# Kernel tuning notes

Measured on AMD Instinct MI355X. Metric: run time of the kernel, lower is better.

## Reference

```python
import jax, jax.numpy as jnp
import numpy as np

N = 50000      # nodes
E = 800000     # edges
IN = 128       # in_channels
H = 128        # hidden_channels
OUT = 40       # out_channels (classes)
EPS = 1e-5     # LayerNorm eps


def _glorot(key, fan_in, fan_out):
    lim = np.sqrt(6.0 / (fan_in + fan_out)).astype(np.float32)
    return jax.random.uniform(key, (fan_in, fan_out), jnp.float32, -lim, lim)


def setup_inputs() -> dict:
    key = jax.random.key(0)
    ks = jax.random.split(key, 8)
    x = jax.random.normal(ks[0], (N, IN), jnp.float32)
    edge_index = jax.random.randint(ks[1], (2, E), 0, N, jnp.int32)
    return {
        "x": x,
        "W0": _glorot(ks[2], IN, H), "b0": jnp.zeros((H,), jnp.float32),
        "W1": _glorot(ks[3], H, H),  "b1": jnp.zeros((H,), jnp.float32),
        "W2": _glorot(ks[4], H, OUT), "b2": jnp.zeros((OUT,), jnp.float32),
        "ln1_g": jnp.ones((H,), jnp.float32), "ln1_b": jnp.zeros((H,), jnp.float32),
        "ln2_g": jnp.ones((H,), jnp.float32), "ln2_b": jnp.zeros((H,), jnp.float32),
        "edge_index": edge_index,
    }


def reference(x, W0, b0, W1, b1, W2, b2, ln1_g, ln1_b, ln2_g, ln2_b, edge_index):
    # GCN normalization with self-loops: A_hat = D^-1/2 (A + I) D^-1/2
    self_idx = jnp.arange(N, dtype=edge_index.dtype)
    src = jnp.concatenate([edge_index[0], self_idx])  # [E+N]
    dst = jnp.concatenate([edge_index[1], self_idx])
    deg = jax.ops.segment_sum(jnp.ones_like(src, jnp.float32), dst, num_segments=N)
    dinv = jax.lax.rsqrt(deg)  # deg >= 1 thanks to self-loops
    norm = dinv[src] * dinv[dst]  # [E+N]

    def conv(h, W, b):
        h = h @ W                                  # [N, F] dense GEMM
        msg = h[src] * norm[:, None]               # gather + scale [E+N, F]
        return jax.ops.segment_sum(msg, dst, num_segments=N) + b

    def layernorm(h, g, b):
        mu = jnp.mean(h, axis=-1, keepdims=True)
        var = jnp.mean(jnp.square(h - mu), axis=-1, keepdims=True)
        return (h - mu) * jax.lax.rsqrt(var + EPS) * g + b

    # layer 0 (note: original uses lns[i+1], so lns[0] is never applied)
    h = jax.nn.relu(layernorm(conv(x, W0, b0), ln1_g, ln1_b))
    # dropout is identity in eval mode
    h = jax.nn.relu(layernorm(conv(h, W1, b1), ln2_g, ln2_b))
    h = conv(h, W2, b2)
    return jax.nn.log_softmax(h, axis=-1)
```

## Files before the change

### kernel.cpp

```cpp
#include <hip/hip_runtime.h>
#include <math.h>

typedef __attribute__((ext_vector_type(8))) short bf16x8;
typedef __attribute__((ext_vector_type(4))) float f32x4;
typedef unsigned short u16;

static __device__ __forceinline__ u16 f2bf(float f) {
    unsigned u = __float_as_uint(f);
    unsigned r = (u + 0x7fff + ((u >> 16) & 1)) >> 16;
    return (u16)r;
}
static __device__ __forceinline__ float bf2f(u16 h) {
    return __uint_as_float(((unsigned)h) << 16);
}
static __device__ __forceinline__ float pk_lo(unsigned u) { return __uint_as_float(u << 16); }
static __device__ __forceinline__ float pk_hi(unsigned u) { return __uint_as_float(u & 0xffff0000u); }

__global__ void zero_int_k(int* __restrict__ p, int n) {
    int i = blockIdx.x * 256 + threadIdx.x;
    if (i < n) p[i] = 0;
}
__global__ void count_rank_k(const int* __restrict__ dst, int* __restrict__ counts,
                             int* __restrict__ rank, int e) {
    int i = blockIdx.x * 256 + threadIdx.x;
    if (i < e) rank[i] = atomicAdd(&counts[dst[i]], 1);
}
__global__ __launch_bounds__(1024) void scan1_k(const int* __restrict__ counts,
                                                int* __restrict__ offs,
                                                int* __restrict__ bsum,
                                                float* __restrict__ dinv, int n) {
    __shared__ int ws[16];
    int tid = threadIdx.x;
    int i = blockIdx.x * 1024 + tid;
    int lane = tid & 63, w = tid >> 6;
    int c = (i < n) ? counts[i] : 0;
    if (i < n) dinv[i] = rsqrtf((float)c + 1.0f);
    int s = c;
#pragma unroll
    for (int o = 1; o < 64; o <<= 1) { int t = __shfl_up(s, o); if (lane >= o) s += t; }
    if (lane == 63) ws[w] = s;
    __syncthreads();
    if (w == 0) {
        int x = (lane < 16) ? ws[lane] : 0;
#pragma unroll
        for (int o = 1; o < 16; o <<= 1) { int t = __shfl_up(x, o); if (lane >= o) x += t; }
        if (lane < 16) ws[lane] = x;
    }
    __syncthreads();
    int base = (w > 0) ? ws[w - 1] : 0;
    int incl = base + s;
    if (i < n) offs[i + 1] = incl;
    if (tid == 1023) bsum[blockIdx.x] = incl;
}
__global__ void scan2_k(int* __restrict__ bsum, int nb) {
    int lane = threadIdx.x;
    int v = (lane < nb) ? bsum[lane] : 0;
#pragma unroll
    for (int o = 1; o < 64; o <<= 1) { int t = __shfl_up(v, o); if (lane >= o) v += t; }
    if (lane < nb) bsum[lane] = v;
}
__global__ void scan3_k(int* __restrict__ offs, const int* __restrict__ bsum, int n) {
    int i = blockIdx.x * 256 + threadIdx.x;
    if (i == 0) offs[0] = 0;
    if (i < n) {
        int b = i >> 10;
        offs[i + 1] += (b > 0) ? bsum[b - 1] : 0;
    }
}
__global__ void fill2_k(const int* __restrict__ src, const int* __restrict__ dst,
                        const int* __restrict__ rank, const int* __restrict__ offs,
                        int* __restrict__ csr, int e) {
    int i = blockIdx.x * 256 + threadIdx.x;
    if (i < e) csr[offs[dst[i]] + rank[i]] = src[i];
}

__global__ void pack_all_k(const float* __restrict__ W0, const float* __restrict__ W1,
                           const float* __restrict__ W2,
                           u16* __restrict__ w0hi, u16* __restrict__ w0lo,
                           u16* __restrict__ w1hi, u16* __restrict__ w1lo,
                           u16* __restrict__ w2hi, u16* __restrict__ w2lo) {
    int i = blockIdx.x * 256 + threadIdx.x;
    const float* W; u16 *hi, *lo; int COLS, cin, idx;
    if (i < 16384)      { W = W0; hi = w0hi; lo = w0lo; COLS = 128; cin = 128; idx = i; }
    else if (i < 32768) { W = W1; hi = w1hi; lo = w1lo; COLS = 128; cin = 128; idx = i - 16384; }
    else if (i < 40960) { W = W2; hi = w2hi; lo = w2lo; COLS = 64;  cin = 40;  idx = i - 32768; }
    else return;
    int k = idx / COLS, col = idx % COLS;
    float v = (col < cin) ? W[k * cin + col] : 0.f;
    u16 h = f2bf(v);
    u16 l = f2bf(v - bf2f(h));
    int ct = col >> 4, ks = k >> 5, ln = (col & 15) + (((k >> 3) & 3) << 4), j = k & 7;
    int pos = (((ct * 4 + ks) * 64 + ln) << 3) + j;
    hi[pos] = h; lo[pos] = l;
}

template<int COLS>
__global__ __launch_bounds__(256) void mfma_gemm_f32a_k(const float* __restrict__ A,
                                                        const u16* __restrict__ Whi,
                                                        const u16* __restrict__ Wlo,
                                                        const float* __restrict__ dinv,
                                                        u16* __restrict__ C, int nrows) {
    int wave = threadIdx.x >> 6, lane = threadIdx.x & 63;
    int r0 = blockIdx.x * 64 + wave * 16;
    int arow = min(r0 + (lane & 15), nrows - 1);
    int kbase = (lane >> 4) * 8;

    bf16x8 ahi[4], alo[4];
#pragma unroll
    for (int ks = 0; ks < 4; ++ks) {
        const float* ap = &A[(long)arow * 128 + ks * 32 + kbase];
        float4 f0 = *(const float4*)ap;
        float4 f1 = *(const float4*)(ap + 4);
        float fv[8] = {f0.x, f0.y, f0.z, f0.w, f1.x, f1.y, f1.z, f1.w};
#pragma unroll
        for (int j = 0; j < 8; ++j) {
            u16 h = f2bf(fv[j]);
            ahi[ks][j] = (short)h;
            alo[ks][j] = (short)f2bf(fv[j] - bf2f(h));
        }
    }
    float dscale[4];
#pragma unroll
    for (int r = 0; r < 4; ++r) {
        int orow = r0 + (lane >> 4) * 4 + r;
        dscale[r] = (orow < nrows) ? dinv[orow] : 0.f;
    }
#pragma unroll
    for (int ct = 0; ct < COLS / 16; ct += 2) {
        f32x4 acc0 = {0.f, 0.f, 0.f, 0.f}, acc1 = {0.f, 0.f, 0.f, 0.f};
#pragma unroll
        for (int ks = 0; ks < 4; ++ks) {
            int fo0 = ((ct * 4 + ks) * 64 + lane) * 8;
            int fo1 = (((ct + 1) * 4 + ks) * 64 + lane) * 8;
            bf16x8 bhi0 = *(const bf16x8*)&Whi[fo0];
            bf16x8 blo0 = *(const bf16x8*)&Wlo[fo0];
            bf16x8 bhi1 = *(const bf16x8*)&Whi[fo1];
            bf16x8 blo1 = *(const bf16x8*)&Wlo[fo1];
            acc0 = __builtin_amdgcn_mfma_f32_16x16x32_bf16(ahi[ks], bhi0, acc0, 0, 0, 0);
            acc1 = __builtin_amdgcn_mfma_f32_16x16x32_bf16(ahi[ks], bhi1, acc1, 0, 0, 0);
            acc0 = __builtin_amdgcn_mfma_f32_16x16x32_bf16(alo[ks], bhi0, acc0, 0, 0, 0);
            acc1 = __builtin_amdgcn_mfma_f32_16x16x32_bf16(alo[ks], bhi1, acc1, 0, 0, 0);
            acc0 = __builtin_amdgcn_mfma_f32_16x16x32_bf16(ahi[ks], blo0, acc0, 0, 0, 0);
            acc1 = __builtin_amdgcn_mfma_f32_16x16x32_bf16(ahi[ks], blo1, acc1, 0, 0, 0);
        }
#pragma unroll
        for (int r = 0; r < 4; ++r) {
            int orow = r0 + (lane >> 4) * 4 + r;
            if (orow < nrows) {
                C[(long)orow * COLS + ct * 16 + (lane & 15)] = f2bf(acc0[r] * dscale[r]);
                C[(long)orow * COLS + (ct + 1) * 16 + (lane & 15)] = f2bf(acc1[r] * dscale[r]);
            }
        }
    }
}

template<int COLS>
__global__ __launch_bounds__(256) void mfma_gemm_bf16a_k(const u16* __restrict__ A,
                                                         const u16* __restrict__ Whi,
                                                         const u16* __restrict__ Wlo,
                                                         const float* __restrict__ dinv,
                                                         u16* __restrict__ C, int nrows) {
    int wave = threadIdx.x >> 6, lane = threadIdx.x & 63;
    int r0 = blockIdx.x * 64 + wave * 16;
    int arow = min(r0 + (lane & 15), nrows - 1);
    int kbase = (lane >> 4) * 8;

    bf16x8 a[4];
#pragma unroll
    for (int ks = 0; ks < 4; ++ks)
        a[ks] = *(const bf16x8*)&A[(long)arow * 128 + ks * 32 + kbase];

    float dscale[4];
#pragma unroll
    for (int r = 0; r < 4; ++r) {
        int orow = r0 + (lane >> 4) * 4 + r;
        dscale[r] = (orow < nrows) ? dinv[orow] : 0.f;
    }
#pragma unroll
    for (int ct = 0; ct < COLS / 16; ct += 2) {
        f32x4 acc0 = {0.f, 0.f, 0.f, 0.f}, acc1 = {0.f, 0.f, 0.f, 0.f};
#pragma unroll
        for (int ks = 0; ks < 4; ++ks) {
            int fo0 = ((ct * 4 + ks) * 64 + lane) * 8;
            int fo1 = (((ct + 1) * 4 + ks) * 64 + lane) * 8;
            bf16x8 bhi0 = *(const bf16x8*)&Whi[fo0];
            bf16x8 blo0 = *(const bf16x8*)&Wlo[fo0];
            bf16x8 bhi1 = *(const bf16x8*)&Whi[fo1];
            bf16x8 blo1 = *(const bf16x8*)&Wlo[fo1];
            acc0 = __builtin_amdgcn_mfma_f32_16x16x32_bf16(a[ks], bhi0, acc0, 0, 0, 0);
            acc1 = __builtin_amdgcn_mfma_f32_16x16x32_bf16(a[ks], bhi1, acc1, 0, 0, 0);
            acc0 = __builtin_amdgcn_mfma_f32_16x16x32_bf16(a[ks], blo0, acc0, 0, 0, 0);
            acc1 = __builtin_amdgcn_mfma_f32_16x16x32_bf16(a[ks], blo1, acc1, 0, 0, 0);
        }
#pragma unroll
        for (int r = 0; r < 4; ++r) {
            int orow = r0 + (lane >> 4) * 4 + r;
            if (orow < nrows) {
                C[(long)orow * COLS + ct * 16 + (lane & 15)] = f2bf(acc0[r] * dscale[r]);
                C[(long)orow * COLS + (ct + 1) * 16 + (lane & 15)] = f2bf(acc1[r] * dscale[r]);
            }
        }
    }
}

__global__ __launch_bounds__(256) void agg_ln_relu_k(const u16* __restrict__ Cs,
                                                     const int* __restrict__ offs,
                                                     const int* __restrict__ csr,
                                                     const float* __restrict__ dinv,
                                                     const float* __restrict__ bias,
                                                     const float* __restrict__ g,
                                                     const float* __restrict__ b,
                                                     u16* __restrict__ out, int n) {
    int wid = (blockIdx.x * 256 + threadIdx.x) >> 6;
    int lane = threadIdx.x & 63;
    if (wid >= n) return;
    const unsigned* C2 = (const unsigned*)Cs;
    unsigned su = C2[(long)wid * 64 + lane];
    float ax = pk_lo(su), ay = pk_hi(su), bx2 = 0.f, by2 = 0.f;
    int beg = offs[wid], end = offs[wid + 1];
    int j = beg;
    while (j < end) {
        int take = min(64, end - j);
        int myidx = (lane < take) ? csr[j + lane] : 0;
        int k = 0;
        for (; k + 8 <= take; k += 8) {
            int i0 = __shfl(myidx, k),     i1 = __shfl(myidx, k + 1);
            int i2 = __shfl(myidx, k + 2), i3 = __shfl(myidx, k + 3);
            int i4 = __shfl(myidx, k + 4), i5 = __shfl(myidx, k + 5);
            int i6 = __shfl(myidx, k + 6), i7 = __shfl(myidx, k + 7);
            unsigned u0 = C2[(long)i0 * 64 + lane], u1 = C2[(long)i1 * 64 + lane];
            unsigned u2 = C2[(long)i2 * 64 + lane], u3 = C2[(long)i3 * 64 + lane];
            unsigned u4 = C2[(long)i4 * 64 + lane], u5 = C2[(long)i5 * 64 + lane];
            unsigned u6 = C2[(long)i6 * 64 + lane], u7 = C2[(long)i7 * 64 + lane];
            ax += pk_lo(u0) + pk_lo(u1) + pk_lo(u2) + pk_lo(u3);
            ay += pk_hi(u0) + pk_hi(u1) + pk_hi(u2) + pk_hi(u3);
            bx2 += pk_lo(u4) + pk_lo(u5) + pk_lo(u6) + pk_lo(u7);
            by2 += pk_hi(u4) + pk_hi(u5) + pk_hi(u6) + pk_hi(u7);
        }
        for (; k < take; ++k) {
            int i0 = __shfl(myidx, k);
            unsigned u0 = C2[(long)i0 * 64 + lane];
            ax += pk_lo(u0); ay += pk_hi(u0);
        }
        j += take;
    }
    float w = dinv[wid];
    float2 bia = ((const float2*)bias)[lane];
    float t0 = (ax + bx2) * w + bia.x;
    float t1 = (ay + by2) * w + bia.y;
    float s = t0 + t1;
#pragma unroll
    for (int off = 32; off; off >>= 1) s += __shfl_xor(s, off);
    float mu = s * (1.f / 128.f);
    float d0 = t0 - mu, d1 = t1 - mu;
    float v = d0 * d0 + d1 * d1;
#pragma unroll
    for (int off = 32; off; off >>= 1) v += __shfl_xor(v, off);
    float rstd = rsqrtf(v * (1.f / 128.f) + 1e-5f);
    float2 gv = ((const float2*)g)[lane];
    float2 bv = ((const float2*)b)[lane];
    float y0 = fmaxf(0.f, d0 * rstd * gv.x + bv.x);
    float y1 = fmaxf(0.f, d1 * rstd * gv.y + bv.y);
    ((unsigned*)out)[(long)wid * 64 + lane] = ((unsigned)f2bf(y1) << 16) | f2bf(y0);
}

__global__ __launch_bounds__(256) void agg_lsm_k(const u16* __restrict__ Cs,
                                                 const int* __restrict__ offs,
                                                 const int* __restrict__ csr,
                                                 const float* __restrict__ dinv,
                                                 const float* __restrict__ b2,
                                                 float* __restrict__ out, int n) {
    int wid = (blockIdx.x * 256 + threadIdx.x) >> 6;
    int lane = threadIdx.x & 63;
    if (wid >= n) return;
    float aa = bf2f(Cs[(long)wid * 64 + lane]), ab = 0.f;
    int beg = offs[wid], end = offs[wid + 1];
    int j = beg;
    while (j < end) {
        int take = min(64, end - j);
        int myidx = (lane < take) ? csr[j + lane] : 0;
        int k = 0;
        for (; k + 8 <= take; k += 8) {
            int i0 = __shfl(myidx, k),     i1 = __shfl(myidx, k + 1);
            int i2 = __shfl(myidx, k + 2), i3 = __shfl(myidx, k + 3);
            int i4 = __shfl(myidx, k + 4), i5 = __shfl(myidx, k + 5);
            int i6 = __shfl(myidx, k + 6), i7 = __shfl(myidx, k + 7);
            float v0 = bf2f(Cs[(long)i0 * 64 + lane]), v1 = bf2f(Cs[(long)i1 * 64 + lane]);
            float v2 = bf2f(Cs[(long)i2 * 64 + lane]), v3 = bf2f(Cs[(long)i3 * 64 + lane]);
            float v4 = bf2f(Cs[(long)i4 * 64 + lane]), v5 = bf2f(Cs[(long)i5 * 64 + lane]);
            float v6 = bf2f(Cs[(long)i6 * 64 + lane]), v7 = bf2f(Cs[(long)i7 * 64 + lane]);
            aa += v0 + v1 + v2 + v3;
            ab += v4 + v5 + v6 + v7;
        }
        for (; k < take; ++k) {
            int i0 = __shfl(myidx, k);
            aa += bf2f(Cs[(long)i0 * 64 + lane]);
        }
        j += take;
    }
    float v = (lane < 40) ? (aa + ab) * dinv[wid] + b2[lane] : -INFINITY;
    float m = v;
#pragma unroll
    for (int off = 32; off; off >>= 1) m = fmaxf(m, __shfl_xor(m, off));
    float e = (lane < 40) ? expf(v - m) : 0.f;
    float s = e;
#pragma unroll
    for (int off = 32; off; off >>= 1) s += __shfl_xor(s, off);
    float r = v - m - logf(s);
    if (lane < 40) out[(long)wid * 40 + lane] = r;
}

extern "C" void kernel_launch(void* const* d_in, const int* in_sizes, int n_in,
                              void* d_out, int out_size, void* d_ws, size_t ws_size,
                              hipStream_t stream) {
    const float* x    = (const float*)d_in[0];
    const float* W0   = (const float*)d_in[1];
    const float* b0   = (const float*)d_in[2];
    const float* W1   = (const float*)d_in[3];
    const float* b1   = (const float*)d_in[4];
    const float* W2   = (const float*)d_in[5];
    const float* b2   = (const float*)d_in[6];
    const float* ln1g = (const float*)d_in[7];
    const float* ln1b = (const float*)d_in[8];
    const float* ln2g = (const float*)d_in[9];
    const float* ln2b = (const float*)d_in[10];
    const int*   ei   = (const int*)d_in[11];

    const int N = in_sizes[0] / 128;
    const int E = in_sizes[11] / 2;
    const int* esrc = ei;
    const int* edst = ei + E;
    float* out = (float*)d_out;

    const int Npad = ((N + 255) / 256) * 256;

    int* counts = (int*)d_ws;
    int* offs   = counts + Npad;
    int* rank   = offs + Npad;
    int* bsum   = rank + E;
    int* csr    = bsum + 64;
    float* dinv = (float*)(csr + E);
    u16* bufA   = (u16*)(dinv + Npad);
    u16* bufB   = bufA + (long)N * 128;
    u16* w0hi   = bufB + (long)N * 128;
    u16* w0lo   = w0hi + 16384;
    u16* w1hi   = w0lo + 16384;
    u16* w1lo   = w1hi + 16384;
    u16* w2hi   = w1lo + 16384;
    u16* w2lo   = w2hi + 8192;

    dim3 blk(256);
    int gN = (N + 255) / 256, gE = (E + 255) / 256;
    int nb1024 = (N + 1023) / 1024;

    zero_int_k<<<gN, blk, 0, stream>>>(counts, N);
    count_rank_k<<<gE, blk, 0, stream>>>(edst, counts, rank, E);
    scan1_k<<<nb1024, 1024, 0, stream>>>(counts, offs, bsum, dinv, N);
    scan2_k<<<1, 64, 0, stream>>>(bsum, nb1024);
    scan3_k<<<gN, blk, 0, stream>>>(offs, bsum, N);
    fill2_k<<<gE, blk, 0, stream>>>(esrc, edst, rank, offs, csr, E);

    pack_all_k<<<160, blk, 0, stream>>>(W0, W1, W2, w0hi, w0lo, w1hi, w1lo, w2hi, w2lo);

    int gG = (N + 63) / 64;
    mfma_gemm_f32a_k<128><<<gG, blk, 0, stream>>>(x, w0hi, w0lo, dinv, bufA, N);
    agg_ln_relu_k<<<(N + 3) / 4, blk, 0, stream>>>(bufA, offs, csr, dinv, b0, ln1g, ln1b, bufB, N);
    mfma_gemm_bf16a_k<128><<<gG, blk, 0, stream>>>(bufB, w1hi, w1lo, dinv, bufA, N);
    agg_ln_relu_k<<<(N + 3) / 4, blk, 0, stream>>>(bufA, offs, csr, dinv, b1, ln2g, ln2b, bufB, N);
    mfma_gemm_bf16a_k<64><<<gG, blk, 0, stream>>>(bufB, w2hi, w2lo, dinv, bufA, N);
    agg_lsm_k<<<(N + 3) / 4, blk, 0, stream>>>(bufA, offs, csr, dinv, b2, out, N);
}
```

Baseline: 213.9 us.

## Slice GEMM outputs by column, aggregate per slice, fuse LayerNorm into next GEMM

GEMM outputs are now stored in column-sliced layout (8 slices of 16 or 8 bf16 columns), so that each aggregation block gathers only a narrow slice per neighbor. The goal is better cache locality for the random-access gather. LayerNorm, bias and ReLU move from the aggregation kernel into the prologue of the following GEMM, and a small kernel applies log-softmax at the end. CSR indices and ranks are shrunk to 16-bit to cut index traffic, which assumes N fits in 65536 (true for 50000). The aggregated sum is rounded to bf16 before normalization, which adds some rounding error.

```diff
diff --git a/kernel.cpp b/kernel.cpp
--- a/kernel.cpp
+++ b/kernel.cpp
@@ -4,6 +4,7 @@
 typedef __attribute__((ext_vector_type(8))) short bf16x8;
 typedef __attribute__((ext_vector_type(4))) float f32x4;
 typedef unsigned short u16;
+typedef unsigned int u32;
 
 static __device__ __forceinline__ u16 f2bf(float f) {
     unsigned u = __float_as_uint(f);
@@ -13,17 +14,17 @@
 static __device__ __forceinline__ float bf2f(u16 h) {
     return __uint_as_float(((unsigned)h) << 16);
 }
-static __device__ __forceinline__ float pk_lo(unsigned u) { return __uint_as_float(u << 16); }
-static __device__ __forceinline__ float pk_hi(unsigned u) { return __uint_as_float(u & 0xffff0000u); }
+static __device__ __forceinline__ float pk_lo(u32 u) { return __uint_as_float(u << 16); }
+static __device__ __forceinline__ float pk_hi(u32 u) { return __uint_as_float(u & 0xffff0000u); }
 
 __global__ void zero_int_k(int* __restrict__ p, int n) {
     int i = blockIdx.x * 256 + threadIdx.x;
     if (i < n) p[i] = 0;
 }
 __global__ void count_rank_k(const int* __restrict__ dst, int* __restrict__ counts,
-                             int* __restrict__ rank, int e) {
-    int i = blockIdx.x * 256 + threadIdx.x;
-    if (i < e) rank[i] = atomicAdd(&counts[dst[i]], 1);
+                             u16* __restrict__ rank, int e) {
+    int i = blockIdx.x * 256 + threadIdx.x;
+    if (i < e) rank[i] = (u16)atomicAdd(&counts[dst[i]], 1);
 }
 __global__ __launch_bounds__(1024) void scan1_k(const int* __restrict__ counts,
                                                 int* __restrict__ offs,
@@ -68,10 +69,10 @@
     }
 }
 __global__ void fill2_k(const int* __restrict__ src, const int* __restrict__ dst,
-                        const int* __restrict__ rank, const int* __restrict__ offs,
-                        int* __restrict__ csr, int e) {
-    int i = blockIdx.x * 256 + threadIdx.x;
-    if (i < e) csr[offs[dst[i]] + rank[i]] = src[i];
+                        const u16* __restrict__ rank, const int* __restrict__ offs,
+                        u16* __restrict__ csr, int e) {
+    int i = blockIdx.x * 256 + threadIdx.x;
+    if (i < e) csr[offs[dst[i]] + (int)rank[i]] = (u16)src[i];
 }
 
 __global__ void pack_all_k(const float* __restrict__ W0, const float* __restrict__ W1,
@@ -92,6 +93,13 @@
     int ct = col >> 4, ks = k >> 5, ln = (col & 15) + (((k >> 3) & 3) << 4), j = k & 7;
     int pos = (((ct * 4 + ks) * 64 + ln) << 3) + j;
     hi[pos] = h; lo[pos] = l;
+}
+
+template<int COLS>
+static __device__ __forceinline__ void store_slice(u16* C, int N, int row, int c, float v) {
+    constexpr int SH = (COLS == 128) ? 4 : 3;
+    constexpr int SC = 1 << SH;
+    C[((size_t)(c >> SH) * N + row) * SC + (c & (SC - 1))] = f2bf(v);
 }
 
 template<int COLS>
@@ -147,28 +155,70 @@
         for (int r = 0; r < 4; ++r) {
             int orow = r0 + (lane >> 4) * 4 + r;
             if (orow < nrows) {
-                C[(long)orow * COLS + ct * 16 + (lane & 15)] = f2bf(acc0[r] * dscale[r]);
-                C[(long)orow * COLS + (ct + 1) * 16 + (lane & 15)] = f2bf(acc1[r] * dscale[r]);
+                store_slice<COLS>(C, nrows, orow, ct * 16 + (lane & 15), acc0[r] * dscale[r]);
+                store_slice<COLS>(C, nrows, orow, (ct + 1) * 16 + (lane & 15), acc1[r] * dscale[r]);
             }
         }
     }
 }
 
 template<int COLS>
-__global__ __launch_bounds__(256) void mfma_gemm_bf16a_k(const u16* __restrict__ A,
-                                                         const u16* __restrict__ Whi,
-                                                         const u16* __restrict__ Wlo,
-                                                         const float* __restrict__ dinv,
-                                                         u16* __restrict__ C, int nrows) {
+__global__ __launch_bounds__(256) void gemm_ln_k(const u32* __restrict__ agg,
+                                                 const u16* __restrict__ Whi,
+                                                 const u16* __restrict__ Wlo,
+                                                 const float* __restrict__ dinv,
+                                                 const float* __restrict__ bias,
+                                                 const float* __restrict__ g,
+                                                 const float* __restrict__ b,
+                                                 u16* __restrict__ C, int nrows) {
     int wave = threadIdx.x >> 6, lane = threadIdx.x & 63;
     int r0 = blockIdx.x * 64 + wave * 16;
     int arow = min(r0 + (lane & 15), nrows - 1);
-    int kbase = (lane >> 4) * 8;
-
-    bf16x8 a[4];
+    int kb = lane >> 4;
+
+    const u32* ap = agg + (size_t)arow * 64 + kb * 4;
+    float dA = dinv[arow];
+    float tv[4][8];
+    float ssum = 0.f;
+#pragma unroll
+    for (int ks = 0; ks < 4; ++ks) {
+#pragma unroll
+        for (int w2 = 0; w2 < 4; ++w2) {
+            u32 u = ap[ks * 16 + w2];
+            int wi = ks * 16 + kb * 4 + w2;
+            float2 bi = ((const float2*)bias)[wi];
+            float t0 = pk_lo(u) * dA + bi.x;
+            float t1 = pk_hi(u) * dA + bi.y;
+            tv[ks][w2 * 2] = t0; tv[ks][w2 * 2 + 1] = t1;
+            ssum += t0 + t1;
+        }
+    }
+    ssum += __shfl_xor(ssum, 16);
+    ssum += __shfl_xor(ssum, 32);
+    float mu = ssum * (1.f / 128.f);
+    float ssq = 0.f;
 #pragma unroll
     for (int ks = 0; ks < 4; ++ks)
-        a[ks] = *(const bf16x8*)&A[(long)arow * 128 + ks * 32 + kbase];
+#pragma unroll
+        for (int j = 0; j < 8; ++j) { float d = tv[ks][j] - mu; ssq += d * d; }
+    ssq += __shfl_xor(ssq, 16);
+    ssq += __shfl_xor(ssq, 32);
+    float rstd = rsqrtf(ssq * (1.f / 128.f) + 1e-5f);
+
+    bf16x8 afr[4];
+#pragma unroll
+    for (int ks = 0; ks < 4; ++ks) {
+#pragma unroll
+        for (int w2 = 0; w2 < 4; ++w2) {
+            int wi = ks * 16 + kb * 4 + w2;
+            float2 gv = ((const float2*)g)[wi];
+            float2 bv = ((const float2*)b)[wi];
+            float y0 = fmaxf(0.f, (tv[ks][w2 * 2] - mu) * rstd * gv.x + bv.x);
+            float y1 = fmaxf(0.f, (tv[ks][w2 * 2 + 1] - mu) * rstd * gv.y + bv.y);
+            afr[ks][w2 * 2] = (short)f2bf(y0);
+            afr[ks][w2 * 2 + 1] = (short)f2bf(y1);
+        }
+    }
 
     float dscale[4];
 #pragma unroll
@@ -187,127 +237,86 @@
             bf16x8 blo0 = *(const bf16x8*)&Wlo[fo0];
             bf16x8 bhi1 = *(const bf16x8*)&Whi[fo1];
             bf16x8 blo1 = *(const bf16x8*)&Wlo[fo1];
-            acc0 = __builtin_amdgcn_mfma_f32_16x16x32_bf16(a[ks], bhi0, acc0, 0, 0, 0);
-            acc1 = __builtin_amdgcn_mfma_f32_16x16x32_bf16(a[ks], bhi1, acc1, 0, 0, 0);
-            acc0 = __builtin_amdgcn_mfma_f32_16x16x32_bf16(a[ks], blo0, acc0, 0, 0, 0);
-            acc1 = __builtin_amdgcn_mfma_f32_16x16x32_bf16(a[ks], blo1, acc1, 0, 0, 0);
+            acc0 = __builtin_amdgcn_mfma_f32_16x16x32_bf16(afr[ks], bhi0, acc0, 0, 0, 0);
+            acc1 = __builtin_amdgcn_mfma_f32_16x16x32_bf16(afr[ks], bhi1, acc1, 0, 0, 0);
+            acc0 = __builtin_amdgcn_mfma_f32_16x16x32_bf16(afr[ks], blo0, acc0, 0, 0, 0);
+            acc1 = __builtin_amdgcn_mfma_f32_16x16x32_bf16(afr[ks], blo1, acc1, 0, 0, 0);
         }
 #pragma unroll
         for (int r = 0; r < 4; ++r) {
             int orow = r0 + (lane >> 4) * 4 + r;
             if (orow < nrows) {
-                C[(long)orow * COLS + ct * 16 + (lane & 15)] = f2bf(acc0[r] * dscale[r]);
-                C[(long)orow * COLS + (ct + 1) * 16 + (lane & 15)] = f2bf(acc1[r] * dscale[r]);
+                store_slice<COLS>(C, nrows, orow, ct * 16 + (lane & 15), acc0[r] * dscale[r]);
+                store_slice<COLS>(C, nrows, orow, (ct + 1) * 16 + (lane & 15), acc1[r] * dscale[r]);
             }
         }
     }
 }
 
-__global__ __launch_bounds__(256) void agg_ln_relu_k(const u16* __restrict__ Cs,
-                                                     const int* __restrict__ offs,
-                                                     const int* __restrict__ csr,
-                                                     const float* __restrict__ dinv,
-                                                     const float* __restrict__ bias,
-                                                     const float* __restrict__ g,
-                                                     const float* __restrict__ b,
-                                                     u16* __restrict__ out, int n) {
+template<int WS>
+__global__ __launch_bounds__(256) void agg_slice_k(const u32* __restrict__ Csl,
+                                                   const int* __restrict__ offs,
+                                                   const u16* __restrict__ csr,
+                                                   u32* __restrict__ aggout, int n) {
+    int s = blockIdx.x & 7;
+    int node = (blockIdx.x >> 3) * 4 + (threadIdx.x >> 6);
+    if (node >= n) return;
+    int l = threadIdx.x & 63;
+    int w = l & (WS - 1);
+    int t = l / WS;
+    constexpr int SLOTS = 64 / WS;
+    const u32* C = Csl + (size_t)s * n * WS;
+    float ax = 0.f, ay = 0.f;
+    if (l < WS) {
+        u32 u = C[(size_t)node * WS + w];
+        ax = pk_lo(u); ay = pk_hi(u);
+    }
+    int beg = offs[node], end = offs[node + 1];
+    for (int j = beg; j < end; j += 64) {
+        int cnt = min(64, end - j);
+        int idx = (l < cnt) ? (int)csr[j + l] : 0;
+        for (int k = 0; k < cnt; k += SLOTS) {
+            int e = k + t;
+            int src = __shfl(idx, e);
+            if (e < cnt) {
+                u32 u = C[(size_t)src * WS + w];
+                ax += pk_lo(u); ay += pk_hi(u);
+            }
+        }
+    }
+#pragma unroll
+    for (int m = WS; m < 64; m <<= 1) {
+        ax += __shfl_xor(ax, m);
+        ay += __shfl_xor(ay, m);
+    }
+    if (l < WS)
+        aggout[(size_t)node * (8 * WS) + s * WS + w] = ((u32)f2bf(ay) << 16) | (u32)f2bf(ax);
+}
+
+__global__ __launch_bounds__(256) void lsm2_k(const u32* __restrict__ agg3,
+                                              const float* __restrict__ dinv,
+                                              const float* __restrict__ b2,
+                                              float* __restrict__ out, int n) {
     int wid = (blockIdx.x * 256 + threadIdx.x) >> 6;
     int lane = threadIdx.x & 63;
     if (wid >= n) return;
-    const unsigned* C2 = (const unsigned*)Cs;
-    unsigned su = C2[(long)wid * 64 + lane];
-    float ax = pk_lo(su), ay = pk_hi(su), bx2 = 0.f, by2 = 0.f;
-    int beg = offs[wid], end = offs[wid + 1];
-    int j = beg;
-    while (j < end) {
-        int take = min(64, end - j);
-        int myidx = (lane < take) ? csr[j + lane] : 0;
-        int k = 0;
-        for (; k + 8 <= take; k += 8) {
-            int i0 = __shfl(myidx, k),     i1 = __shfl(myidx, k + 1);
-            int i2 = __shfl(myidx, k + 2), i3 = __shfl(myidx, k + 3);
-            int i4 = __shfl(myidx, k + 4), i5 = __shfl(myidx, k + 5);
-            int i6 = __shfl(myidx, k + 6), i7 = __shfl(myidx, k + 7);
-            unsigned u0 = C2[(long)i0 * 64 + lane], u1 = C2[(long)i1 * 64 + lane];
-            unsigned u2 = C2[(long)i2 * 64 + lane], u3 = C2[(long)i3 * 64 + lane];
-            unsigned u4 = C2[(long)i4 * 64 + lane], u5 = C2[(long)i5 * 64 + lane];
-            unsigned u6 = C2[(long)i6 * 64 + lane], u7 = C2[(long)i7 * 64 + lane];
-            ax += pk_lo(u0) + pk_lo(u1) + pk_lo(u2) + pk_lo(u3);
-            ay += pk_hi(u0) + pk_hi(u1) + pk_hi(u2) + pk_hi(u3);
-            bx2 += pk_lo(u4) + pk_lo(u5) + pk_lo(u6) + pk_lo(u7);
-            by2 += pk_hi(u4) + pk_hi(u5) + pk_hi(u6) + pk_hi(u7);
-        }
-        for (; k < take; ++k) {
-            int i0 = __shfl(myidx, k);
-            unsigned u0 = C2[(long)i0 * 64 + lane];
-            ax += pk_lo(u0); ay += pk_hi(u0);
-        }
-        j += take;
-    }
-    float w = dinv[wid];
-    float2 bia = ((const float2*)bias)[lane];
-    float t0 = (ax + bx2) * w + bia.x;
-    float t1 = (ay + by2) * w + bia.y;
-    float s = t0 + t1;
-#pragma unroll
-    for (int off = 32; off; off >>= 1) s += __shfl_xor(s, off);
-    float mu = s * (1.f / 128.f);
-    float d0 = t0 - mu, d1 = t1 - mu;
-    float v = d0 * d0 + d1 * d1;
-#pragma unroll
-    for (int off = 32; off; off >>= 1) v += __shfl_xor(v, off);
-    float rstd = rsqrtf(v * (1.f / 128.f) + 1e-5f);
-    float2 gv = ((const float2*)g)[lane];
-    float2 bv = ((const float2*)b)[lane];
-    float y0 = fmaxf(0.f, d0 * rstd * gv.x + bv.x);
-    float y1 = fmaxf(0.f, d1 * rstd * gv.y + bv.y);
-    ((unsigned*)out)[(long)wid * 64 + lane] = ((unsigned)f2bf(y1) << 16) | f2bf(y0);
-}
-
-__global__ __launch_bounds__(256) void agg_lsm_k(const u16* __restrict__ Cs,
-                                                 const int* __restrict__ offs,
-                                                 const int* __restrict__ csr,
-                                                 const float* __restrict__ dinv,
-                                                 const float* __restrict__ b2,
-                                                 float* __restrict__ out, int n) {
-    int wid = (blockIdx.x * 256 + threadIdx.x) >> 6;
-    int lane = threadIdx.x & 63;
-    if (wid >= n) return;
-    float aa = bf2f(Cs[(long)wid * 64 + lane]), ab = 0.f;
-    int beg = offs[wid], end = offs[wid + 1];
-    int j = beg;
-    while (j < end) {
-        int take = min(64, end - j);
-        int myidx = (lane < take) ? csr[j + lane] : 0;
-        int k = 0;
-        for (; k + 8 <= take; k += 8) {
-            int i0 = __shfl(myidx, k),     i1 = __shfl(myidx, k + 1);
-            int i2 = __shfl(myidx, k + 2), i3 = __shfl(myidx, k + 3);
-            int i4 = __shfl(myidx, k + 4), i5 = __shfl(myidx, k + 5);
-            int i6 = __shfl(myidx, k + 6), i7 = __shfl(myidx, k + 7);
-            float v0 = bf2f(Cs[(long)i0 * 64 + lane]), v1 = bf2f(Cs[(long)i1 * 64 + lane]);
-            float v2 = bf2f(Cs[(long)i2 * 64 + lane]), v3 = bf2f(Cs[(long)i3 * 64 + lane]);
-            float v4 = bf2f(Cs[(long)i4 * 64 + lane]), v5 = bf2f(Cs[(long)i5 * 64 + lane]);
-            float v6 = bf2f(Cs[(long)i6 * 64 + lane]), v7 = bf2f(Cs[(long)i7 * 64 + lane]);
-            aa += v0 + v1 + v2 + v3;
-            ab += v4 + v5 + v6 + v7;
-        }
-        for (; k < take; ++k) {
-            int i0 = __shfl(myidx, k);
-            aa += bf2f(Cs[(long)i0 * 64 + lane]);
-        }
-        j += take;
-    }
-    float v = (lane < 40) ? (aa + ab) * dinv[wid] + b2[lane] : -INFINITY;
-    float m = v;
+    float v0 = -INFINITY, v1 = -INFINITY;
+    if (lane < 20) {
+        u32 u = agg3[(size_t)wid * 32 + lane];
+        float dA = dinv[wid];
+        float2 bb = ((const float2*)b2)[lane];
+        v0 = pk_lo(u) * dA + bb.x;
+        v1 = pk_hi(u) * dA + bb.y;
+    }
+    float m = fmaxf(v0, v1);
 #pragma unroll
     for (int off = 32; off; off >>= 1) m = fmaxf(m, __shfl_xor(m, off));
-    float e = (lane < 40) ? expf(v - m) : 0.f;
-    float s = e;
-#pragma unroll
-    for (int off = 32; off; off >>= 1) s += __shfl_xor(s, off);
-    float r = v - m - logf(s);
-    if (lane < 40) out[(long)wid * 40 + lane] = r;
+    float e = (lane < 20) ? (expf(v0 - m) + expf(v1 - m)) : 0.f;
+#pragma unroll
+    for (int off = 32; off; off >>= 1) e += __shfl_xor(e, off);
+    float ls = logf(e);
+    if (lane < 20)
+        ((float2*)out)[(size_t)wid * 20 + lane] = make_float2(v0 - m - ls, v1 - m - ls);
 }
 
 extern "C" void kernel_launch(void* const* d_in, const int* in_sizes, int n_in,
@@ -334,39 +343,42 @@
 
     const int Npad = ((N + 255) / 256) * 256;
 
-    int* counts = (int*)d_ws;
-    int* offs   = counts + Npad;
-    int* rank   = offs + Npad;
-    int* bsum   = rank + E;
-    int* csr    = bsum + 64;
-    float* dinv = (float*)(csr + E);
-    u16* bufA   = (u16*)(dinv + Npad);
-    u16* bufB   = bufA + (long)N * 128;
-    u16* w0hi   = bufB + (long)N * 128;
-    u16* w0lo   = w0hi + 16384;
-    u16* w1hi   = w0lo + 16384;
-    u16* w1lo   = w1hi + 16384;
-    u16* w2hi   = w1lo + 16384;
-    u16* w2lo   = w2hi + 8192;
+    int* counts  = (int*)d_ws;
+    int* offs    = counts + Npad;
+    int* bsum    = offs + Npad;
+    u16* rank16  = (u16*)(bsum + 64);
+    u16* csr16   = rank16 + E;
+    float* dinv  = (float*)(csr16 + E);
+    u16* bufC    = (u16*)(dinv + Npad);
+    u32* bufAgg  = (u32*)(bufC + (size_t)N * 128);
+    u16* w0hi    = (u16*)(bufAgg + (size_t)N * 64);
+    u16* w0lo    = w0hi + 16384;
+    u16* w1hi    = w0lo + 16384;
+    u16* w1lo    = w1hi + 16384;
+    u16* w2hi    = w1lo + 16384;
+    u16* w2lo    = w2hi + 8192;
 
     dim3 blk(256);
     int gN = (N + 255) / 256, gE = (E + 255) / 256;
     int nb1024 = (N + 1023) / 1024;
+    int gG = (N + 63) / 64;
+    int gA = ((N + 3) / 4) * 8;
+    int gW = (N + 3) / 4;
 
     zero_int_k<<<gN, blk, 0, stream>>>(counts, N);
-    count_rank_k<<<gE, blk, 0, stream>>>(edst, counts, rank, E);
+    count_rank_k<<<gE, blk, 0, stream>>>(edst, counts, rank16, E);
     scan1_k<<<nb1024, 1024, 0, stream>>>(counts, offs, bsum, dinv, N);
     scan2_k<<<1, 64, 0, stream>>>(bsum, nb1024);
     scan3_k<<<gN, blk, 0, stream>>>(offs, bsum, N);
-    fill2_k<<<gE, blk, 0, stream>>>(esrc, edst, rank, offs, csr, E);
+    fill2_k<<<gE, blk, 0, stream>>>(esrc, edst, rank16, offs, csr16, E);
 
     pack_all_k<<<160, blk, 0, stream>>>(W0, W1, W2, w0hi, w0lo, w1hi, w1lo, w2hi, w2lo);
 
-    int gG = (N + 63) / 64;
-    mfma_gemm_f32a_k<128><<<gG, blk, 0, stream>>>(x, w0hi, w0lo, dinv, bufA, N);
-    agg_ln_relu_k<<<(N + 3) / 4, blk, 0, stream>>>(bufA, offs, csr, dinv, b0, ln1g, ln1b, bufB, N);
-    mfma_gemm_bf16a_k<128><<<gG, blk, 0, stream>>>(bufB, w1hi, w1lo, dinv, bufA, N);
-    agg_ln_relu_k<<<(N + 3) / 4, blk, 0, stream>>>(bufA, offs, csr, dinv, b1, ln2g, ln2b, bufB, N);
-    mfma_gemm_bf16a_k<64><<<gG, blk, 0, stream>>>(bufB, w2hi, w2lo, dinv, bufA, N);
-    agg_lsm_k<<<(N + 3) / 4, blk, 0, stream>>>(bufA, offs, csr, dinv, b2, out, N);
-}
+    mfma_gemm_f32a_k<128><<<gG, blk, 0, stream>>>(x, w0hi, w0lo, dinv, bufC, N);
+    agg_slice_k<8><<<gA, blk, 0, stream>>>((const u32*)bufC, offs, csr16, bufAgg, N);
+    gemm_ln_k<128><<<gG, blk, 0, stream>>>(bufAgg, w1hi, w1lo, dinv, b0, ln1g, ln1b, bufC, N);
+    agg_slice_k<8><<<gA, blk, 0, stream>>>((const u32*)bufC, offs, csr16, bufAgg, N);
+    gemm_ln_k<64><<<gG, blk, 0, stream>>>(bufAgg, w2hi, w2lo, dinv, b1, ln2g, ln2b, bufC, N);
+    agg_slice_k<4><<<gA, blk, 0, stream>>>((const u32*)bufC, offs, csr16, bufAgg, N);
+    lsm2_k<<<gW, blk, 0, stream>>>(bufAgg, dinv, b2, out, N);
+}
```

Measured after the change: 430.2 us. +101.2%, slower.

## Fuse setup kernels, merge CSR fill with first GEMM, use 16-bit CSR indices

Applied to the files above, without the earlier changes.

Merges the zeroing and weight-packing kernels into one launch, and folds scan2 into scan3. The CSR fill and the first-layer GEMM now run in a single launch as disjoint block ranges. The rank and CSR arrays are stored as 16-bit values, halving index traffic in the three aggregation kernels. This relies on the node count fitting in 16 bits and on no node having more than 65535 in-edges. Each scan23 block also recomputes the 64-entry block-sum prefix redundantly.

```diff
diff --git a/kernel.cpp b/kernel.cpp
--- a/kernel.cpp
+++ b/kernel.cpp
@@ -4,6 +4,7 @@
 typedef __attribute__((ext_vector_type(8))) short bf16x8;
 typedef __attribute__((ext_vector_type(4))) float f32x4;
 typedef unsigned short u16;
+typedef unsigned int u32;
 
 static __device__ __forceinline__ u16 f2bf(float f) {
     unsigned u = __float_as_uint(f);
@@ -13,73 +14,22 @@
 static __device__ __forceinline__ float bf2f(u16 h) {
     return __uint_as_float(((unsigned)h) << 16);
 }
-static __device__ __forceinline__ float pk_lo(unsigned u) { return __uint_as_float(u << 16); }
-static __device__ __forceinline__ float pk_hi(unsigned u) { return __uint_as_float(u & 0xffff0000u); }
-
-__global__ void zero_int_k(int* __restrict__ p, int n) {
-    int i = blockIdx.x * 256 + threadIdx.x;
-    if (i < n) p[i] = 0;
-}
-__global__ void count_rank_k(const int* __restrict__ dst, int* __restrict__ counts,
-                             int* __restrict__ rank, int e) {
-    int i = blockIdx.x * 256 + threadIdx.x;
-    if (i < e) rank[i] = atomicAdd(&counts[dst[i]], 1);
-}
-__global__ __launch_bounds__(1024) void scan1_k(const int* __restrict__ counts,
-                                                int* __restrict__ offs,
-                                                int* __restrict__ bsum,
-                                                float* __restrict__ dinv, int n) {
-    __shared__ int ws[16];
-    int tid = threadIdx.x;
-    int i = blockIdx.x * 1024 + tid;
-    int lane = tid & 63, w = tid >> 6;
-    int c = (i < n) ? counts[i] : 0;
-    if (i < n) dinv[i] = rsqrtf((float)c + 1.0f);
-    int s = c;
-#pragma unroll
-    for (int o = 1; o < 64; o <<= 1) { int t = __shfl_up(s, o); if (lane >= o) s += t; }
-    if (lane == 63) ws[w] = s;
-    __syncthreads();
-    if (w == 0) {
-        int x = (lane < 16) ? ws[lane] : 0;
-#pragma unroll
-        for (int o = 1; o < 16; o <<= 1) { int t = __shfl_up(x, o); if (lane >= o) x += t; }
-        if (lane < 16) ws[lane] = x;
-    }
-    __syncthreads();
-    int base = (w > 0) ? ws[w - 1] : 0;
-    int incl = base + s;
-    if (i < n) offs[i + 1] = incl;
-    if (tid == 1023) bsum[blockIdx.x] = incl;
-}
-__global__ void scan2_k(int* __restrict__ bsum, int nb) {
-    int lane = threadIdx.x;
-    int v = (lane < nb) ? bsum[lane] : 0;
-#pragma unroll
-    for (int o = 1; o < 64; o <<= 1) { int t = __shfl_up(v, o); if (lane >= o) v += t; }
-    if (lane < nb) bsum[lane] = v;
-}
-__global__ void scan3_k(int* __restrict__ offs, const int* __restrict__ bsum, int n) {
-    int i = blockIdx.x * 256 + threadIdx.x;
-    if (i == 0) offs[0] = 0;
-    if (i < n) {
-        int b = i >> 10;
-        offs[i + 1] += (b > 0) ? bsum[b - 1] : 0;
-    }
-}
-__global__ void fill2_k(const int* __restrict__ src, const int* __restrict__ dst,
-                        const int* __restrict__ rank, const int* __restrict__ offs,
-                        int* __restrict__ csr, int e) {
-    int i = blockIdx.x * 256 + threadIdx.x;
-    if (i < e) csr[offs[dst[i]] + rank[i]] = src[i];
-}
-
-__global__ void pack_all_k(const float* __restrict__ W0, const float* __restrict__ W1,
-                           const float* __restrict__ W2,
-                           u16* __restrict__ w0hi, u16* __restrict__ w0lo,
-                           u16* __restrict__ w1hi, u16* __restrict__ w1lo,
-                           u16* __restrict__ w2hi, u16* __restrict__ w2lo) {
-    int i = blockIdx.x * 256 + threadIdx.x;
+static __device__ __forceinline__ float pk_lo(u32 u) { return __uint_as_float(u << 16); }
+static __device__ __forceinline__ float pk_hi(u32 u) { return __uint_as_float(u & 0xffff0000u); }
+
+__global__ void init_k(int* __restrict__ counts, int n, int gN,
+                       const float* __restrict__ W0, const float* __restrict__ W1,
+                       const float* __restrict__ W2,
+                       u16* __restrict__ w0hi, u16* __restrict__ w0lo,
+                       u16* __restrict__ w1hi, u16* __restrict__ w1lo,
+                       u16* __restrict__ w2hi, u16* __restrict__ w2lo) {
+    int b = blockIdx.x;
+    if (b < gN) {
+        int i = b * 256 + threadIdx.x;
+        if (i < n) counts[i] = 0;
+        return;
+    }
+    int i = (b - gN) * 256 + threadIdx.x;
     const float* W; u16 *hi, *lo; int COLS, cin, idx;
     if (i < 16384)      { W = W0; hi = w0hi; lo = w0lo; COLS = 128; cin = 128; idx = i; }
     else if (i < 32768) { W = W1; hi = w1hi; lo = w1lo; COLS = 128; cin = 128; idx = i - 16384; }
@@ -94,14 +44,76 @@
     hi[pos] = h; lo[pos] = l;
 }
 
-template<int COLS>
-__global__ __launch_bounds__(256) void mfma_gemm_f32a_k(const float* __restrict__ A,
-                                                        const u16* __restrict__ Whi,
-                                                        const u16* __restrict__ Wlo,
-                                                        const float* __restrict__ dinv,
-                                                        u16* __restrict__ C, int nrows) {
+__global__ void count_rank_k(const int* __restrict__ dst, int* __restrict__ counts,
+                             u16* __restrict__ rank, int e) {
+    int i = blockIdx.x * 256 + threadIdx.x;
+    if (i < e) rank[i] = (u16)atomicAdd(&counts[dst[i]], 1);
+}
+__global__ __launch_bounds__(1024) void scan1_k(const int* __restrict__ counts,
+                                                int* __restrict__ offs,
+                                                int* __restrict__ bsum,
+                                                float* __restrict__ dinv, int n) {
+    __shared__ int ws[16];
+    int tid = threadIdx.x;
+    int i = blockIdx.x * 1024 + tid;
+    int lane = tid & 63, w = tid >> 6;
+    int c = (i < n) ? counts[i] : 0;
+    if (i < n) dinv[i] = rsqrtf((float)c + 1.0f);
+    int s = c;
+#pragma unroll
+    for (int o = 1; o < 64; o <<= 1) { int t = __shfl_up(s, o); if (lane >= o) s += t; }
+    if (lane == 63) ws[w] = s;
+    __syncthreads();
+    if (w == 0) {
+        int x = (lane < 16) ? ws[lane] : 0;
+#pragma unroll
+        for (int o = 1; o < 16; o <<= 1) { int t = __shfl_up(x, o); if (lane >= o) x += t; }
+        if (lane < 16) ws[lane] = x;
+    }
+    __syncthreads();
+    int base = (w > 0) ? ws[w - 1] : 0;
+    int incl = base + s;
+    if (i < n) offs[i + 1] = incl;
+    if (tid == 1023) bsum[blockIdx.x] = incl;
+}
+__global__ void scan23_k(int* __restrict__ offs, const int* __restrict__ bsum,
+                         int nb, int n) {
+    __shared__ int pre[64];
+    int tid = threadIdx.x;
+    if (tid < 64) {
+        int v = (tid < nb) ? bsum[tid] : 0;
+#pragma unroll
+        for (int o = 1; o < 64; o <<= 1) { int t = __shfl_up(v, o); if (tid >= o) v += t; }
+        pre[tid] = v;
+    }
+    __syncthreads();
+    int i = blockIdx.x * 256 + tid;
+    if (i == 0) offs[0] = 0;
+    if (i < n) {
+        int b = i >> 10;
+        offs[i + 1] += (b > 0) ? pre[b - 1] : 0;
+    }
+}
+
+__global__ __launch_bounds__(256) void fill_gemm1_k(const int* __restrict__ src,
+                                                    const int* __restrict__ dst,
+                                                    const u16* __restrict__ rank,
+                                                    const int* __restrict__ offs,
+                                                    u16* __restrict__ csr, int e, int fillBlocks,
+                                                    const float* __restrict__ A,
+                                                    const u16* __restrict__ Whi,
+                                                    const u16* __restrict__ Wlo,
+                                                    const float* __restrict__ dinv,
+                                                    u16* __restrict__ C, int nrows) {
+    if ((int)blockIdx.x < fillBlocks) {
+        int i = blockIdx.x * 256 + threadIdx.x;
+        if (i < e) csr[offs[dst[i]] + (int)rank[i]] = (u16)src[i];
+        return;
+    }
+    constexpr int COLS = 128;
+    int bid = blockIdx.x - fillBlocks;
     int wave = threadIdx.x >> 6, lane = threadIdx.x & 63;
-    int r0 = blockIdx.x * 64 + wave * 16;
+    int r0 = bid * 64 + wave * 16;
     int arow = min(r0 + (lane & 15), nrows - 1);
     int kbase = (lane >> 4) * 8;
 
@@ -205,7 +217,7 @@
 
 __global__ __launch_bounds__(256) void agg_ln_relu_k(const u16* __restrict__ Cs,
                                                      const int* __restrict__ offs,
-                                                     const int* __restrict__ csr,
+                                                     const u16* __restrict__ csr,
                                                      const float* __restrict__ dinv,
                                                      const float* __restrict__ bias,
                                                      const float* __restrict__ g,
@@ -214,24 +226,24 @@
     int wid = (blockIdx.x * 256 + threadIdx.x) >> 6;
     int lane = threadIdx.x & 63;
     if (wid >= n) return;
-    const unsigned* C2 = (const unsigned*)Cs;
-    unsigned su = C2[(long)wid * 64 + lane];
+    const u32* C2 = (const u32*)Cs;
+    u32 su = C2[(long)wid * 64 + lane];
     float ax = pk_lo(su), ay = pk_hi(su), bx2 = 0.f, by2 = 0.f;
     int beg = offs[wid], end = offs[wid + 1];
     int j = beg;
     while (j < end) {
         int take = min(64, end - j);
-        int myidx = (lane < take) ? csr[j + lane] : 0;
+        int myidx = (lane < take) ? (int)csr[j + lane] : 0;
         int k = 0;
         for (; k + 8 <= take; k += 8) {
             int i0 = __shfl(myidx, k),     i1 = __shfl(myidx, k + 1);
             int i2 = __shfl(myidx, k + 2), i3 = __shfl(myidx, k + 3);
             int i4 = __shfl(myidx, k + 4), i5 = __shfl(myidx, k + 5);
             int i6 = __shfl(myidx, k + 6), i7 = __shfl(myidx, k + 7);
-            unsigned u0 = C2[(long)i0 * 64 + lane], u1 = C2[(long)i1 * 64 + lane];
-            unsigned u2 = C2[(long)i2 * 64 + lane], u3 = C2[(long)i3 * 64 + lane];
-            unsigned u4 = C2[(long)i4 * 64 + lane], u5 = C2[(long)i5 * 64 + lane];
-            unsigned u6 = C2[(long)i6 * 64 + lane], u7 = C2[(long)i7 * 64 + lane];
+            u32 u0 = C2[(long)i0 * 64 + lane], u1 = C2[(long)i1 * 64 + lane];
+            u32 u2 = C2[(long)i2 * 64 + lane], u3 = C2[(long)i3 * 64 + lane];
+            u32 u4 = C2[(long)i4 * 64 + lane], u5 = C2[(long)i5 * 64 + lane];
+            u32 u6 = C2[(long)i6 * 64 + lane], u7 = C2[(long)i7 * 64 + lane];
             ax += pk_lo(u0) + pk_lo(u1) + pk_lo(u2) + pk_lo(u3);
             ay += pk_hi(u0) + pk_hi(u1) + pk_hi(u2) + pk_hi(u3);
             bx2 += pk_lo(u4) + pk_lo(u5) + pk_lo(u6) + pk_lo(u7);
@@ -239,7 +251,7 @@
         }
         for (; k < take; ++k) {
             int i0 = __shfl(myidx, k);
-            unsigned u0 = C2[(long)i0 * 64 + lane];
+            u32 u0 = C2[(long)i0 * 64 + lane];
             ax += pk_lo(u0); ay += pk_hi(u0);
         }
         j += take;
@@ -261,12 +273,12 @@
     float2 bv = ((const float2*)b)[lane];
     float y0 = fmaxf(0.f, d0 * rstd * gv.x + bv.x);
     float y1 = fmaxf(0.f, d1 * rstd * gv.y + bv.y);
-    ((unsigned*)out)[(long)wid * 64 + lane] = ((unsigned)f2bf(y1) << 16) | f2bf(y0);
+    ((u32*)out)[(long)wid * 64 + lane] = ((u32)f2bf(y1) << 16) | f2bf(y0);
 }
 
 __global__ __launch_bounds__(256) void agg_lsm_k(const u16* __restrict__ Cs,
                                                  const int* __restrict__ offs,
-                                                 const int* __restrict__ csr,
+                                                 const u16* __restrict__ csr,
                                                  const float* __restrict__ dinv,
                                                  const float* __restrict__ b2,
                                                  float* __restrict__ out, int n) {
@@ -278,7 +290,7 @@
     int j = beg;
     while (j < end) {
         int take = min(64, end - j);
-        int myidx = (lane < take) ? csr[j + lane] : 0;
+        int myidx = (lane < take) ? (int)csr[j + lane] : 0;
         int k = 0;
         for (; k + 8 <= take; k += 8) {
             int i0 = __shfl(myidx, k),     i1 = __shfl(myidx, k + 1);
@@ -334,39 +346,37 @@
 
     const int Npad = ((N + 255) / 256) * 256;
 
-    int* counts = (int*)d_ws;
-    int* offs   = counts + Npad;
-    int* rank   = offs + Npad;
-    int* bsum   = rank + E;
-    int* csr    = bsum + 64;
-    float* dinv = (float*)(csr + E);
-    u16* bufA   = (u16*)(dinv + Npad);
-    u16* bufB   = bufA + (long)N * 128;
-    u16* w0hi   = bufB + (long)N * 128;
-    u16* w0lo   = w0hi + 16384;
-    u16* w1hi   = w0lo + 16384;
-    u16* w1lo   = w1hi + 16384;
-    u16* w2hi   = w1lo + 16384;
-    u16* w2lo   = w2hi + 8192;
+    int* counts  = (int*)d_ws;
+    int* offs    = counts + Npad;
+    int* bsum    = offs + Npad;
+    u16* rank16  = (u16*)(bsum + 64);
+    u16* csr16   = rank16 + E;
+    float* dinv  = (float*)(csr16 + E);
+    u16* bufA    = (u16*)(dinv + Npad);
+    u16* bufB    = bufA + (size_t)N * 128;
+    u16* w0hi    = bufB + (size_t)N * 128;
+    u16* w0lo    = w0hi + 16384;
+    u16* w1hi    = w0lo + 16384;
+    u16* w1lo    = w1hi + 16384;
+    u16* w2hi    = w1lo + 16384;
+    u16* w2lo    = w2hi + 8192;
 
     dim3 blk(256);
     int gN = (N + 255) / 256, gE = (E + 255) / 256;
     int nb1024 = (N + 1023) / 1024;
-
-    zero_int_k<<<gN, blk, 0, stream>>>(counts, N);
-    count_rank_k<<<gE, blk, 0, stream>>>(edst, counts, rank, E);
+    int gG = (N + 63) / 64;
+    int gW = (N + 3) / 4;
+
+    init_k<<<gN + 160, blk, 0, stream>>>(counts, N, gN, W0, W1, W2,
+                                         w0hi, w0lo, w1hi, w1lo, w2hi, w2lo);
+    count_rank_k<<<gE, blk, 0, stream>>>(edst, counts, rank16, E);
     scan1_k<<<nb1024, 1024, 0, stream>>>(counts, offs, bsum, dinv, N);
-    scan2_k<<<1, 64, 0, stream>>>(bsum, nb1024);
-    scan3_k<<<gN, blk, 0, stream>>>(offs, bsum, N);
-    fill2_k<<<gE, blk, 0, stream>>>(esrc, edst, rank, offs, csr, E);
-
-    pack_all_k<<<160, blk, 0, stream>>>(W0, W1, W2, w0hi, w0lo, w1hi, w1lo, w2hi, w2lo);
-
-    int gG = (N + 63) / 64;
-    mfma_gemm_f32a_k<128><<<gG, blk, 0, stream>>>(x, w0hi, w0lo, dinv, bufA, N);
-    agg_ln_relu_k<<<(N + 3) / 4, blk, 0, stream>>>(bufA, offs, csr, dinv, b0, ln1g, ln1b, bufB, N);
+    scan23_k<<<gN, blk, 0, stream>>>(offs, bsum, nb1024, N);
+    fill_gemm1_k<<<gE + gG, blk, 0, stream>>>(esrc, edst, rank16, offs, csr16, E, gE,
+                                              x, w0hi, w0lo, dinv, bufA, N);
+    agg_ln_relu_k<<<gW, blk, 0, stream>>>(bufA, offs, csr16, dinv, b0, ln1g, ln1b, bufB, N);
     mfma_gemm_bf16a_k<128><<<gG, blk, 0, stream>>>(bufB, w1hi, w1lo, dinv, bufA, N);
-    agg_ln_relu_k<<<(N + 3) / 4, blk, 0, stream>>>(bufA, offs, csr, dinv, b1, ln2g, ln2b, bufB, N);
+    agg_ln_relu_k<<<gW, blk, 0, stream>>>(bufA, offs, csr16, dinv, b1, ln2g, ln2b, bufB, N);
     mfma_gemm_bf16a_k<64><<<gG, blk, 0, stream>>>(bufB, w2hi, w2lo, dinv, bufA, N);
-    agg_lsm_k<<<(N + 3) / 4, blk, 0, stream>>>(bufA, offs, csr, dinv, b2, out, N);
-}
+    agg_lsm_k<<<gW, blk, 0, stream>>>(bufA, offs, csr16, dinv, b2, out, N);
+}
```

Result: faster. 207.1 us (-3.2%).
